# Optimization experiments

Hardware: AMD Instinct MI355X
Metric: run time of the kernel (lower is better)

Reference implementation:

```python
import jax, jax.numpy as jnp
import numpy as np

F = 1024
H = 16
DH = F // H  # 64
MLP = 4096
EPS = 1e-5


def layernorm(x, g, b):
    mu = x.mean(-1, keepdims=True)
    var = ((x - mu) ** 2).mean(-1, keepdims=True)
    return (x - mu) * jax.lax.rsqrt(var + EPS) * g + b


def softmax_off_by_one(a):
    e = jnp.exp(a - a.max(-1, keepdims=True))
    return e / (1.0 + e.sum(-1, keepdims=True))


def setup_inputs() -> dict:
    key = jax.random.key(0)
    ks = jax.random.split(key, 12)
    s = 0.02
    return {
        "x": jax.random.normal(ks[0], (2, 2048, F), jnp.float32),
        "ln1_g": jnp.ones((F,), jnp.float32),
        "ln1_b": jnp.zeros((F,), jnp.float32),
        "Wq": jax.random.normal(ks[1], (F, F), jnp.float32) * s,
        "bq": jnp.zeros((F,), jnp.float32),
        "Wk": jax.random.normal(ks[2], (F, F), jnp.float32) * s,
        "bk": jnp.zeros((F,), jnp.float32),
        "Wv": jax.random.normal(ks[3], (F, F), jnp.float32) * s,
        "bv": jnp.zeros((F,), jnp.float32),
        "Wo": jax.random.normal(ks[4], (F, F), jnp.float32) * s,
        "bo": jnp.zeros((F,), jnp.float32),
        "slim": jnp.ones((H,), jnp.float32),
        "ln2_g": jnp.ones((F,), jnp.float32),
        "ln2_b": jnp.zeros((F,), jnp.float32),
        "W1": jax.random.normal(ks[5], (F, MLP), jnp.float32) * s,
        "b1": jnp.zeros((MLP,), jnp.float32),
        "W2": jax.random.normal(ks[6], (MLP, F), jnp.float32) * s,
        "b2": jnp.zeros((F,), jnp.float32),
    }


def reference(x, ln1_g, ln1_b, Wq, bq, Wk, bk, Wv, bv, Wo, bo, slim,
              ln2_g, ln2_b, W1, b1, W2, b2):
    b, n, f = x.shape
    h = layernorm(x, ln1_g, ln1_b)
    # project and split heads: [b, H, n, DH]
    q = (h @ Wq + bq).reshape(b, n, H, DH).transpose(0, 2, 1, 3)
    k = (h @ Wk + bk).reshape(b, n, H, DH).transpose(0, 2, 1, 3)
    v = (h @ Wv + bv).reshape(b, n, H, DH).transpose(0, 2, 1, 3)
    att = jnp.einsum('bhid,bhjd->bhij', q, k) / (DH ** 0.5)
    probs = softmax_off_by_one(att)  # off-by-one softmax
    probs = probs * slim[None, :, None, None]  # slimming after softmax
    attn = jnp.einsum('bhij,bhjd->bihd', probs, v).reshape(b, n, F)
    out = attn @ Wo + bo + x  # residual 1
    h2 = layernorm(out, ln2_g, ln2_b)
    m = jax.nn.gelu(h2 @ W1 + b1, approximate=False)
    m = jax.nn.gelu(m @ W2 + b2, approximate=False)
    return m + out  # residual 2
```

## Files before the change

kernel.cpp:

```cpp
#include <hip/hip_runtime.h>
#include <hip/hip_bf16.h>

typedef __hip_bfloat16 bf16;
typedef short bf16x8 __attribute__((ext_vector_type(8)));
typedef float f32x4 __attribute__((ext_vector_type(4)));

__device__ __forceinline__ float gelu_f(float x) {
  return 0.5f * x * (1.f + erff(x * 0.70710678118654752f));
}

__device__ __forceinline__ unsigned short f2bfu(float f) {
  bf16 h = __float2bfloat16(f);
  unsigned short u;
  __builtin_memcpy(&u, &h, 2);
  return u;
}

__device__ __forceinline__ void load16_lds(const bf16* g, bf16* l) {
  __builtin_amdgcn_global_load_lds(
      (const __attribute__((address_space(1))) unsigned int*)g,
      (__attribute__((address_space(3))) unsigned int*)l, 16, 0, 0);
}

__global__ __launch_bounds__(256) void transpose_cast(
    const float* __restrict__ src, bf16* __restrict__ dst, int R, int C) {
  __shared__ float tile[32][33];
  int tx = threadIdx.x & 31, ty = threadIdx.x >> 5;
  int r0 = blockIdx.y * 32, c0 = blockIdx.x * 32;
  #pragma unroll
  for (int i = ty; i < 32; i += 8)
    tile[i][tx] = src[(size_t)(r0 + i) * C + (c0 + tx)];
  __syncthreads();
  #pragma unroll
  for (int i = ty; i < 32; i += 8)
    dst[(size_t)(c0 + i) * R + (r0 + tx)] = __float2bfloat16(tile[tx][i]);
}

__global__ __launch_bounds__(256) void ln_kernel(
    const float* __restrict__ x, const float* __restrict__ g,
    const float* __restrict__ b, bf16* __restrict__ y) {
  int row = blockIdx.x;
  int t = threadIdx.x;
  const float4* xr = (const float4*)(x + (size_t)row * 1024);
  float4 v = xr[t];
  float s = v.x + v.y + v.z + v.w;
  float ss = v.x * v.x + v.y * v.y + v.z * v.z + v.w * v.w;
  #pragma unroll
  for (int off = 32; off >= 1; off >>= 1) {
    s += __shfl_xor(s, off);
    ss += __shfl_xor(ss, off);
  }
  __shared__ float red[8];
  int wv = t >> 6;
  if ((t & 63) == 0) { red[wv] = s; red[4 + wv] = ss; }
  __syncthreads();
  float S = red[0] + red[1] + red[2] + red[3];
  float SS = red[4] + red[5] + red[6] + red[7];
  float mu = S * (1.f / 1024.f);
  float var = SS * (1.f / 1024.f) - mu * mu;
  float inv = rsqrtf(var + 1e-5f);
  float4 gv = ((const float4*)g)[t];
  float4 bv = ((const float4*)b)[t];
  ushort4 o;
  o.x = f2bfu((v.x - mu) * inv * gv.x + bv.x);
  o.y = f2bfu((v.y - mu) * inv * gv.y + bv.y);
  o.z = f2bfu((v.z - mu) * inv * gv.z + bv.z);
  o.w = f2bfu((v.w - mu) * inv * gv.w + bv.w);
  ((ushort4*)(y + (size_t)row * 1024))[t] = o;
}

template <int EPI>
__global__ __launch_bounds__(256) void gemm_bf16(
    const bf16* __restrict__ A, const bf16* __restrict__ Bt,
    const float* __restrict__ bias0, const float* __restrict__ bias1,
    const float* __restrict__ bias2, const float* __restrict__ resid,
    void* __restrict__ C0, void* __restrict__ C1, void* __restrict__ C2,
    int M, int N, int K) {
  __shared__ __align__(16) bf16 As[2][128 * 32];
  __shared__ __align__(16) bf16 Bs[2][128 * 32];
  const int t = threadIdx.x, lane = t & 63, w = t >> 6;
  const int wm = (w >> 1) * 64, wn = (w & 1) * 64;
  const int m0 = blockIdx.y * 128, n0 = blockIdx.x * 128;

  const int srow = lane >> 2;
  const int sgrp = lane & 3;
  f32x4 acc[4][4] = {};

  const bf16* Abase = A + (size_t)m0 * K;
  const bf16* Bbase = Bt + (size_t)n0 * K;

  auto stage = [&](int buf, int kt) {
    #pragma unroll
    for (int c = 0; c < 2; ++c) {
      int row = w * 32 + c * 16 + srow;
      int sw = (row & 3) ^ ((row >> 2) & 3);
      int gg = sgrp ^ sw;
      const bf16* ga = Abase + (size_t)row * K + kt + gg * 8;
      const bf16* gb = Bbase + (size_t)row * K + kt + gg * 8;
      load16_lds(ga, &As[buf][(w * 32 + c * 16) * 32]);
      load16_lds(gb, &Bs[buf][(w * 32 + c * 16) * 32]);
    }
  };

  const int q8 = (((lane >> 4) ^ (lane & 3) ^ ((lane >> 2) & 3))) * 8;
  const int fr = lane & 15;

  const int nk = K >> 5;
  stage(0, 0);
  for (int i = 0; i < nk; ++i) {
    const int cur = i & 1;
    __syncthreads();
    if (i + 1 < nk) stage(cur ^ 1, (i + 1) << 5);
    bf16x8 af[4], bfr[4];
    #pragma unroll
    for (int mc = 0; mc < 4; ++mc)
      af[mc] = *(const bf16x8*)&As[cur][(wm + mc * 16 + fr) * 32 + q8];
    #pragma unroll
    for (int nc = 0; nc < 4; ++nc)
      bfr[nc] = *(const bf16x8*)&Bs[cur][(wn + nc * 16 + fr) * 32 + q8];
    #pragma unroll
    for (int mc = 0; mc < 4; ++mc)
      #pragma unroll
      for (int nc = 0; nc < 4; ++nc)
        acc[mc][nc] = __builtin_amdgcn_mfma_f32_16x16x32_bf16(
            af[mc], bfr[nc], acc[mc][nc], 0, 0, 0);
  }

  if constexpr (EPI == 0) {
    const int which = n0 >> 10;
    const float* bp = which == 0 ? bias0 : which == 1 ? bias1 : bias2;
    bf16* qk = (bf16*)(which == 0 ? C0 : C1);
    #pragma unroll
    for (int mc = 0; mc < 4; ++mc) {
      #pragma unroll
      for (int reg = 0; reg < 4; ++reg) {
        int m = m0 + wm + mc * 16 + ((lane >> 4) << 2) + reg;
        int b = m >> 11, tok = m & 2047;
        #pragma unroll
        for (int nc = 0; nc < 4; ++nc) {
          int n = n0 + wn + nc * 16 + (lane & 15);
          int nn = n & 1023, hh = nn >> 6, d = n & 63;
          float val = acc[mc][nc][reg] + bp[nn];
          if (which == 2)
            ((bf16*)C2)[(size_t)((b * 16 + hh) * 64 + d) * 2048 + tok] =
                __float2bfloat16(val);
          else
            qk[(size_t)((b * 16 + hh) * 2048 + tok) * 64 + d] =
                __float2bfloat16(val);
        }
      }
    }
  } else {
    #pragma unroll
    for (int mc = 0; mc < 4; ++mc) {
      #pragma unroll
      for (int reg = 0; reg < 4; ++reg) {
        int m = m0 + wm + mc * 16 + ((lane >> 4) << 2) + reg;
        #pragma unroll
        for (int nc = 0; nc < 4; ++nc) {
          int n = n0 + wn + nc * 16 + (lane & 15);
          float val = acc[mc][nc][reg] + bias0[n];
          size_t idx = (size_t)m * N + n;
          if constexpr (EPI == 3) {
            ((float*)C0)[idx] = val + resid[idx];
          } else if constexpr (EPI == 4) {
            ((bf16*)C0)[idx] = __float2bfloat16(gelu_f(val));
          } else {
            ((float*)C0)[idx] = gelu_f(val) + resid[idx];
          }
        }
      }
    }
  }
}

__global__ __launch_bounds__(256) void attn_kernel(
    const bf16* __restrict__ q, const bf16* __restrict__ k,
    const bf16* __restrict__ vt, const float* __restrict__ slim,
    bf16* __restrict__ attn) {
  __shared__ __align__(16) bf16 Ks[64][64];
  __shared__ __align__(16) bf16 Vs[64][64];
  __shared__ __align__(16) bf16 Ps[4][16][72];

  const int t = threadIdx.x, lane = t & 63, w = t >> 6;
  const int fr = lane & 15, qd = lane >> 4;
  const int bh = blockIdx.y;
  const int q0 = blockIdx.x * 64;
  const size_t bhbase = (size_t)bh * 2048 * 64;

  const int qrow = q0 + w * 16 + fr;
  const bf16* qp = q + bhbase + (size_t)qrow * 64 + qd * 8;
  bf16x8 qf0 = *(const bf16x8*)qp;
  bf16x8 qf1 = *(const bf16x8*)(qp + 32);

  const int srow = lane >> 3;
  const int sg = lane & 7;

  f32x4 o_acc[4] = {};
  float m_lane[4] = {-3.0e38f, -3.0e38f, -3.0e38f, -3.0e38f};
  float l_lane[4] = {0.f, 0.f, 0.f, 0.f};
  const float C = 0.18033688011f;

  for (int j0 = 0; j0 < 2048; j0 += 64) {
    __syncthreads();
    #pragma unroll
    for (int c = 0; c < 2; ++c) {
      int r = w * 16 + c * 8 + srow;
      int gk = sg ^ (r & 7);
      load16_lds(k + bhbase + (size_t)(j0 + r) * 64 + gk * 8, &Ks[w * 16 + c * 8][0]);
      load16_lds(vt + bhbase + (size_t)r * 2048 + j0 + gk * 8, &Vs[w * 16 + c * 8][0]);
    }
    __syncthreads();

    f32x4 z[4];
    #pragma unroll
    for (int nc = 0; nc < 4; ++nc) {
      int kr = nc * 16 + fr;
      bf16x8 kf0 = *(const bf16x8*)&Ks[kr][(qd ^ (kr & 7)) * 8];
      bf16x8 kf1 = *(const bf16x8*)&Ks[kr][((qd + 4) ^ (kr & 7)) * 8];
      f32x4 zz = {};
      zz = __builtin_amdgcn_mfma_f32_16x16x32_bf16(qf0, kf0, zz, 0, 0, 0);
      zz = __builtin_amdgcn_mfma_f32_16x16x32_bf16(qf1, kf1, zz, 0, 0, 0);
      z[nc] = zz;
    }

    #pragma unroll
    for (int nc = 0; nc < 4; ++nc)
      #pragma unroll
      for (int r = 0; r < 4; ++r) {
        float p = exp2f(z[nc][r] * C);
        l_lane[r] += p;
        m_lane[r] = fmaxf(m_lane[r], z[nc][r]);
        Ps[w][qd * 4 + r][nc * 16 + fr] = __float2bfloat16(p);
      }

    bf16x8 pf0 = *(const bf16x8*)&Ps[w][fr][qd * 8];
    bf16x8 pf1 = *(const bf16x8*)&Ps[w][fr][32 + qd * 8];
    #pragma unroll
    for (int dc = 0; dc < 4; ++dc) {
      int vr = dc * 16 + fr;
      bf16x8 vf0 = *(const bf16x8*)&Vs[vr][(qd ^ (vr & 7)) * 8];
      bf16x8 vf1 = *(const bf16x8*)&Vs[vr][((qd + 4) ^ (vr & 7)) * 8];
      o_acc[dc] = __builtin_amdgcn_mfma_f32_16x16x32_bf16(pf0, vf0, o_acc[dc], 0, 0, 0);
      o_acc[dc] = __builtin_amdgcn_mfma_f32_16x16x32_bf16(pf1, vf1, o_acc[dc], 0, 0, 0);
    }
  }

  #pragma unroll
  for (int off = 1; off <= 8; off <<= 1)
    #pragma unroll
    for (int r = 0; r < 4; ++r) {
      l_lane[r] += __shfl_xor(l_lane[r], off);
      m_lane[r] = fmaxf(m_lane[r], __shfl_xor(m_lane[r], off));
    }

  const int b = bh >> 4, hh = bh & 15;
  const float sl = slim[hh];
  #pragma unroll
  for (int r = 0; r < 4; ++r) {
    float inv = sl / (exp2f(m_lane[r] * C) + l_lane[r]);
    int mrow = b * 2048 + q0 + w * 16 + qd * 4 + r;
    #pragma unroll
    for (int dc = 0; dc < 4; ++dc) {
      int col = hh * 64 + dc * 16 + fr;
      attn[(size_t)mrow * 1024 + col] = __float2bfloat16(o_acc[dc][r] * inv);
    }
  }
}

extern "C" void kernel_launch(void* const* d_in, const int* in_sizes, int n_in,
                              void* d_out, int out_size, void* d_ws, size_t ws_size,
                              hipStream_t stream) {
  const float* x    = (const float*)d_in[0];
  const float* ln1g = (const float*)d_in[1];
  const float* ln1b = (const float*)d_in[2];
  const float* Wq   = (const float*)d_in[3];
  const float* bq   = (const float*)d_in[4];
  const float* Wk   = (const float*)d_in[5];
  const float* bk   = (const float*)d_in[6];
  const float* Wv   = (const float*)d_in[7];
  const float* bv   = (const float*)d_in[8];
  const float* Wo   = (const float*)d_in[9];
  const float* bo   = (const float*)d_in[10];
  const float* slim = (const float*)d_in[11];
  const float* ln2g = (const float*)d_in[12];
  const float* ln2b = (const float*)d_in[13];
  const float* W1   = (const float*)d_in[14];
  const float* b1   = (const float*)d_in[15];
  const float* W2   = (const float*)d_in[16];
  const float* b2   = (const float*)d_in[17];

  char* p = (char*)d_ws;
  auto take = [&](size_t nbytes) {
    char* r = p;
    p += (nbytes + 255) & ~(size_t)255;
    return r;
  };
  bf16* Wqkv_t = (bf16*)take((size_t)3072 * 1024 * 2);
  bf16* Wo_t = (bf16*)take((size_t)1024 * 1024 * 2);
  bf16* W1_t = (bf16*)take((size_t)4096 * 1024 * 2);
  bf16* W2_t = (bf16*)take((size_t)1024 * 4096 * 2);
  bf16* h1   = (bf16*)take((size_t)4096 * 1024 * 2);
  bf16* qb   = (bf16*)take((size_t)4096 * 1024 * 2);
  bf16* kb   = (bf16*)take((size_t)4096 * 1024 * 2);
  bf16* vtb  = (bf16*)take((size_t)4096 * 1024 * 2);
  bf16* attn = (bf16*)take((size_t)4096 * 1024 * 2);
  float* out1 = (float*)take((size_t)4096 * 1024 * 4);
  bf16* h2   = (bf16*)take((size_t)4096 * 1024 * 2);
  bf16* m1   = (bf16*)take((size_t)4096 * 4096 * 2);

  dim3 blk(256);

  transpose_cast<<<dim3(32, 32), blk, 0, stream>>>(Wq, Wqkv_t, 1024, 1024);
  transpose_cast<<<dim3(32, 32), blk, 0, stream>>>(Wk, Wqkv_t + (size_t)1024 * 1024, 1024, 1024);
  transpose_cast<<<dim3(32, 32), blk, 0, stream>>>(Wv, Wqkv_t + (size_t)2048 * 1024, 1024, 1024);
  transpose_cast<<<dim3(32, 32), blk, 0, stream>>>(Wo, Wo_t, 1024, 1024);
  transpose_cast<<<dim3(128, 32), blk, 0, stream>>>(W1, W1_t, 1024, 4096);
  transpose_cast<<<dim3(32, 128), blk, 0, stream>>>(W2, W2_t, 4096, 1024);

  ln_kernel<<<4096, blk, 0, stream>>>(x, ln1g, ln1b, h1);

  gemm_bf16<0><<<dim3(24, 32), blk, 0, stream>>>(
      h1, Wqkv_t, bq, bk, bv, nullptr, qb, kb, vtb, 4096, 3072, 1024);

  attn_kernel<<<dim3(32, 32), blk, 0, stream>>>(qb, kb, vtb, slim, attn);

  gemm_bf16<3><<<dim3(8, 32), blk, 0, stream>>>(
      attn, Wo_t, bo, nullptr, nullptr, x, out1, nullptr, nullptr, 4096, 1024, 1024);

  ln_kernel<<<4096, blk, 0, stream>>>(out1, ln2g, ln2b, h2);

  gemm_bf16<4><<<dim3(32, 32), blk, 0, stream>>>(
      h2, W1_t, b1, nullptr, nullptr, nullptr, m1, nullptr, nullptr, 4096, 4096, 1024);
  gemm_bf16<5><<<dim3(8, 32), blk, 0, stream>>>(
      m1, W2_t, b2, nullptr, nullptr, out1, (float*)d_out, nullptr, nullptr, 4096, 1024, 4096);
}
```

Baseline: 463.1 us.

## Split-K the second MLP GEMM into four chunks with a separate reduce kernel

The W2 GEMM (K=4096) is split along K into four 1024-wide chunks using a third grid dimension, so it launches 1024 blocks instead of 256. Each chunk writes bf16 partial sums into dead scratch buffers (h1, q, k, vt). A new reduce kernel then sums the partials and applies bias, GELU and the residual. The aim is more parallelism and occupancy on a GEMM whose grid only matches the CU count. The cost is about 32 MB of extra partial-sum traffic and an extra launch. Storing partials in bf16 also loses some precision.

```diff
diff --git a/kernel.cpp b/kernel.cpp
--- a/kernel.cpp
+++ b/kernel.cpp
@@ -82,12 +82,15 @@
   const int wm = (w >> 1) * 64, wn = (w & 1) * 64;
   const int m0 = blockIdx.y * 128, n0 = blockIdx.x * 128;
 
+  const int koff = (EPI == 6) ? (int)blockIdx.z * 1024 : 0;
+  const int kc_len = (EPI == 6) ? 1024 : K;
+
   const int srow = lane >> 2;
   const int sgrp = lane & 3;
   f32x4 acc[4][4] = {};
 
-  const bf16* Abase = A + (size_t)m0 * K;
-  const bf16* Bbase = Bt + (size_t)n0 * K;
+  const bf16* Abase = A + (size_t)m0 * K + koff;
+  const bf16* Bbase = Bt + (size_t)n0 * K + koff;
 
   auto stage = [&](int buf, int kt) {
     #pragma unroll
@@ -105,7 +108,7 @@
   const int q8 = (((lane >> 4) ^ (lane & 3) ^ ((lane >> 2) & 3))) * 8;
   const int fr = lane & 15;
 
-  const int nk = K >> 5;
+  const int nk = kc_len >> 5;
   stage(0, 0);
   for (int i = 0; i < nk; ++i) {
     const int cur = i & 1;
@@ -150,6 +153,20 @@
         }
       }
     }
+  } else if constexpr (EPI == 6) {
+    bf16* pout = (bf16*)C0 + (size_t)blockIdx.z * M * N;
+    #pragma unroll
+    for (int mc = 0; mc < 4; ++mc) {
+      #pragma unroll
+      for (int reg = 0; reg < 4; ++reg) {
+        int m = m0 + wm + mc * 16 + ((lane >> 4) << 2) + reg;
+        #pragma unroll
+        for (int nc = 0; nc < 4; ++nc) {
+          int n = n0 + wn + nc * 16 + (lane & 15);
+          pout[(size_t)m * N + n] = __float2bfloat16(acc[mc][nc][reg]);
+        }
+      }
+    }
   } else {
     #pragma unroll
     for (int mc = 0; mc < 4; ++mc) {
@@ -172,6 +189,33 @@
       }
     }
   }
+}
+
+__global__ __launch_bounds__(256) void reduce_mlp2(
+    const bf16* __restrict__ part, const float* __restrict__ b2,
+    const float* __restrict__ out1, float* __restrict__ out) {
+  const int row = blockIdx.x, t = threadIdx.x;
+  const size_t base = (size_t)row * 1024 + t * 4;
+  float sum[4] = {0.f, 0.f, 0.f, 0.f};
+  #pragma unroll
+  for (int kc = 0; kc < 4; ++kc) {
+    ushort4 u = *(const ushort4*)(part + (size_t)kc * 4096 * 1024 + base);
+    unsigned short us[4] = {u.x, u.y, u.z, u.w};
+    #pragma unroll
+    for (int j = 0; j < 4; ++j) {
+      bf16 h;
+      __builtin_memcpy(&h, &us[j], 2);
+      sum[j] += __bfloat162float(h);
+    }
+  }
+  float4 bv = ((const float4*)b2)[t];
+  float4 rv = *(const float4*)(out1 + base);
+  float4 o;
+  o.x = gelu_f(sum[0] + bv.x) + rv.x;
+  o.y = gelu_f(sum[1] + bv.y) + rv.y;
+  o.z = gelu_f(sum[2] + bv.z) + rv.z;
+  o.w = gelu_f(sum[3] + bv.w) + rv.w;
+  *(float4*)(out + base) = o;
 }
 
 __global__ __launch_bounds__(256) void attn_kernel(
@@ -309,6 +353,8 @@
   bf16* h2   = (bf16*)take((size_t)4096 * 1024 * 2);
   bf16* m1   = (bf16*)take((size_t)4096 * 4096 * 2);
 
+  bf16* parts = h1;
+
   dim3 blk(256);
 
   transpose_cast<<<dim3(32, 32), blk, 0, stream>>>(Wq, Wqkv_t, 1024, 1024);
@@ -332,6 +378,9 @@
 
   gemm_bf16<4><<<dim3(32, 32), blk, 0, stream>>>(
       h2, W1_t, b1, nullptr, nullptr, nullptr, m1, nullptr, nullptr, 4096, 4096, 1024);
-  gemm_bf16<5><<<dim3(8, 32), blk, 0, stream>>>(
-      m1, W2_t, b2, nullptr, nullptr, out1, (float*)d_out, nullptr, nullptr, 4096, 1024, 4096);
-}
+
+  gemm_bf16<6><<<dim3(8, 32, 4), blk, 0, stream>>>(
+      m1, W2_t, nullptr, nullptr, nullptr, nullptr, parts, nullptr, nullptr,
+      4096, 1024, 4096);
+  reduce_mlp2<<<4096, blk, 0, stream>>>(parts, b2, out1, (float*)d_out);
+}
```

Result: faster. 435.1 us (-6.0%).
